# Optimization experiments

Measured on AMD Instinct MI355X. Metric: run time of the kernel, lower is better.

Reference implementation:

```python
import jax, jax.numpy as jnp
import numpy as np

DIM = 512
HEADS = 8
DIM_HEAD = 64
INNER = HEADS * DIM_HEAD  # 512
EPS = 1e-5


def setup_inputs() -> dict:
    key = jax.random.key(0)
    ks = jax.random.split(key, 8)
    b, n = 4, 2048
    x = jax.random.normal(ks[0], (b, n, DIM), dtype=jnp.float32)
    ln_g = jnp.ones((DIM,), jnp.float32)
    ln_b = jnp.zeros((DIM,), jnp.float32)
    w_qkv = jax.random.normal(ks[1], (DIM, 3 * INNER), jnp.float32) * (DIM ** -0.5)
    reattn_w = jax.random.normal(ks[2], (HEADS, HEADS), jnp.float32)
    rn_g = jnp.ones((HEADS,), jnp.float32)
    rn_b = jnp.zeros((HEADS,), jnp.float32)
    w_out = jax.random.normal(ks[3], (INNER, DIM), jnp.float32) * (INNER ** -0.5)
    b_out = jnp.zeros((DIM,), jnp.float32)
    return {"x": x, "ln_g": ln_g, "ln_b": ln_b, "w_qkv": w_qkv,
            "reattn_w": reattn_w, "rn_g": rn_g, "rn_b": rn_b,
            "w_out": w_out, "b_out": b_out}


def _layernorm(x, g, b, axis=-1):
    mu = jnp.mean(x, axis=axis, keepdims=True)
    var = jnp.var(x, axis=axis, keepdims=True)
    return (x - mu) * jax.lax.rsqrt(var + EPS) * g + b


def reference(x, ln_g, ln_b, w_qkv, reattn_w, rn_g, rn_b, w_out, b_out):
    b, n, _ = x.shape
    h, d = HEADS, DIM_HEAD
    scale = d ** -0.5
    xn = _layernorm(x, ln_g, ln_b)                       # [b,n,dim]
    qkv = xn @ w_qkv                                     # [b,n,3*inner]
    q, k, v = jnp.split(qkv, 3, axis=-1)
    to_heads = lambda t: t.reshape(b, n, h, d).transpose(0, 2, 1, 3)  # [b,h,n,d]
    q, k, v = to_heads(q), to_heads(k), to_heads(v)
    dots = jnp.einsum('bhid,bhjd->bhij', q, k) * scale   # [b,h,n,n]
    attn = jax.nn.softmax(dots, axis=-1)
    # cross-head re-attention mixing
    attn = jnp.einsum('bhij,hg->bgij', attn, reattn_w)
    # LayerNorm over the head axis (axis=1), affine params shaped [h]
    attn = _layernorm(attn, rn_g[None, :, None, None], rn_b[None, :, None, None], axis=1)
    out = jnp.einsum('bhij,bhjd->bhid', attn, v)         # [b,h,n,d]
    out = out.transpose(0, 2, 1, 3).reshape(b, n, h * d)
    return out @ w_out + b_out
```

## Files before the change

kernel.cpp:

```cpp
#include <hip/hip_runtime.h>
#include <hip/hip_bf16.h>
#include <math.h>

#define DEV __device__ __forceinline__

typedef short bf16x8 __attribute__((ext_vector_type(8)));
typedef short bf16x4 __attribute__((ext_vector_type(4)));
typedef float f32x4 __attribute__((ext_vector_type(4)));

static const int Nn = 2048;
static const int DIMd = 512;

DEV float bf2f(short u) {
    union { unsigned int i; float f; } c;
    c.i = ((unsigned int)(unsigned short)u) << 16;
    return c.f;
}

DEV short f2bf(float f) {
    union { float f; unsigned int i; } c;
    c.f = f;
    unsigned int u = c.i;
    unsigned int r = (u + 0x7fffu + ((u >> 16) & 1u)) >> 16;
    return (short)r;
}

DEV void gload16(const short* __restrict__ g, short* l) {
    __builtin_amdgcn_global_load_lds(
        (__attribute__((address_space(1))) void*)g,
        (__attribute__((address_space(3))) void*)l, 16, 0, 0);
}

__global__ void k_transpose_cast(const float* __restrict__ src,
                                 short* __restrict__ dst, int K, int N) {
    int o = blockIdx.x * 256 + threadIdx.x;
    if (o >= K * N) return;
    int n = o / K, k = o - n * K;
    dst[o] = f2bf(src[(size_t)k * N + n]);
}

__global__ __launch_bounds__(256) void k_ln(const float* __restrict__ x,
                                            const float* __restrict__ g,
                                            const float* __restrict__ bta,
                                            short* __restrict__ xn) {
    int row = blockIdx.x * 4 + (threadIdx.x >> 6);
    int lane = threadIdx.x & 63;
    const float* xr = x + (size_t)row * DIMd;
    float4 v0 = ((const float4*)xr)[lane * 2];
    float4 v1 = ((const float4*)xr)[lane * 2 + 1];
    float f[8] = {v0.x, v0.y, v0.z, v0.w, v1.x, v1.y, v1.z, v1.w};
    float s = 0.f, sq = 0.f;
#pragma unroll
    for (int t = 0; t < 8; ++t) { s += f[t]; sq += f[t] * f[t]; }
#pragma unroll
    for (int off = 32; off >= 1; off >>= 1) {
        s += __shfl_xor(s, off);
        sq += __shfl_xor(sq, off);
    }
    float mu = s * (1.0f / 512.0f);
    float var = sq * (1.0f / 512.0f) - mu * mu;
    float rs = rsqrtf(var + 1e-5f);
    bf16x8 o;
#pragma unroll
    for (int t = 0; t < 8; ++t) {
        int c = lane * 8 + t;
        o[t] = f2bf((f[t] - mu) * rs * g[c] + bta[c]);
    }
    *(bf16x8*)(xn + (size_t)row * DIMd + lane * 8) = o;
}

DEV void gemm128_loop(const short* __restrict__ A, const short* __restrict__ B,
                      int K, int i0, int n0, int tid,
                      short* As, short* Bs, f32x4 acc[4][4]) {
    const int w = tid >> 6, wr = w >> 1, wc = w & 1;
    const int lane = tid & 63, fr = lane & 15, fq = lane >> 4;
    const int sr = tid >> 3, sc = (tid & 7) * 8;
    for (int k0 = 0; k0 < K; k0 += 64) {
#pragma unroll
        for (int L = 0; L < 4; ++L) {
            gload16(A + (size_t)(i0 + L * 32 + sr) * K + k0 + sc,
                    As + (L * 32 + sr) * 64 + sc);
            gload16(B + (size_t)(n0 + L * 32 + sr) * K + k0 + sc,
                    Bs + (L * 32 + sr) * 64 + sc);
        }
        __syncthreads();
#pragma unroll
        for (int kk = 0; kk < 2; ++kk) {
            bf16x8 af[4], bfr[4];
#pragma unroll
            for (int m = 0; m < 4; ++m)
                af[m] = *(const bf16x8*)(As + (wr * 64 + m * 16 + fr) * 64 + kk * 32 + fq * 8);
#pragma unroll
            for (int n = 0; n < 4; ++n)
                bfr[n] = *(const bf16x8*)(Bs + (wc * 64 + n * 16 + fr) * 64 + kk * 32 + fq * 8);
#pragma unroll
            for (int m = 0; m < 4; ++m)
#pragma unroll
                for (int n = 0; n < 4; ++n)
                    acc[m][n] = __builtin_amdgcn_mfma_f32_16x16x32_bf16(af[m], bfr[n], acc[m][n], 0, 0, 0);
        }
        __syncthreads();
    }
}

__global__ __launch_bounds__(256) void k_qkv(const short* __restrict__ xn,
                                             const short* __restrict__ wT,
                                             short* __restrict__ Q,
                                             short* __restrict__ Kb,
                                             short* __restrict__ Vt) {
    __shared__ short As[128 * 64], Bs[128 * 64];
    int tid = threadIdx.x;
    int i0 = blockIdx.x * 128, n0 = blockIdx.y * 128;
    f32x4 acc[4][4] = {};
    gemm128_loop(xn, wT, DIMd, i0, n0, tid, As, Bs, acc);
    const int w = tid >> 6, wr = w >> 1, wc = w & 1;
    const int lane = tid & 63, fr = lane & 15, fq = lane >> 4;
#pragma unroll
    for (int m = 0; m < 4; ++m) {
#pragma unroll
        for (int n = 0; n < 4; ++n) {
#pragma unroll
            for (int r = 0; r < 4; ++r) {
                int row = i0 + wr * 64 + m * 16 + fq * 4 + r;
                int c = n0 + wc * 64 + n * 16 + fr;
                float v = acc[m][n][r];
                int b = row >> 11, i = row & 2047;
                int t = c >> 9, rem = c & 511;
                int h = rem >> 6, dd = rem & 63;
                size_t bh = (size_t)(b * 8 + h);
                if (t == 0)      Q [(bh * Nn + i) * 64 + dd] = f2bf(v * 0.125f);
                else if (t == 1) Kb[(bh * Nn + i) * 64 + dd] = f2bf(v);
                else             Vt[(bh * 64 + dd) * Nn + i] = f2bf(v);
            }
        }
    }
}

__global__ __launch_bounds__(256) void k_out(const short* __restrict__ outh,
                                             const short* __restrict__ wT,
                                             const float* __restrict__ bias,
                                             float* __restrict__ out) {
    __shared__ short As[128 * 64], Bs[128 * 64];
    int tid = threadIdx.x;
    int i0 = blockIdx.x * 128, n0 = blockIdx.y * 128;
    f32x4 acc[4][4] = {};
    gemm128_loop(outh, wT, 512, i0, n0, tid, As, Bs, acc);
    const int w = tid >> 6, wr = w >> 1, wc = w & 1;
    const int lane = tid & 63, fr = lane & 15, fq = lane >> 4;
#pragma unroll
    for (int m = 0; m < 4; ++m)
#pragma unroll
        for (int n = 0; n < 4; ++n)
#pragma unroll
            for (int r = 0; r < 4; ++r) {
                int row = i0 + wr * 64 + m * 16 + fq * 4 + r;
                int c = n0 + wc * 64 + n * 16 + fr;
                out[(size_t)row * 512 + c] = acc[m][n][r] + bias[c];
            }
}

DEV void decode_bid2(int bid, int& b, int& i0, int& jh) {
    int xcd = bid & 7, slot = bid >> 3;
    b = xcd >> 1;
    jh = xcd & 1;
    i0 = slot * 32;
}

__global__ __launch_bounds__(512)
__attribute__((amdgpu_waves_per_eu(4, 4)))
void k_stats(const short* __restrict__ Q,
             const short* __restrict__ Kb,
             float* __restrict__ mpart,
             float* __restrict__ lpart) {
    int b, i0, jh;
    decode_bid2(blockIdx.x, b, i0, jh);
    int tid = threadIdx.x, wv = tid >> 6, lane = tid & 63;
    int fr = lane & 15, fq = lane >> 4;
    size_t bh = (size_t)(b * 8 + wv);
    const short* qb = Q + (bh * Nn + i0) * 64;
    bf16x8 qf[2][2];
#pragma unroll
    for (int in = 0; in < 2; ++in)
#pragma unroll
        for (int kk = 0; kk < 2; ++kk)
            qf[in][kk] = *(const bf16x8*)(qb + (in * 16 + fr) * 64 + kk * 32 + fq * 8);
    float m[2] = {-1e30f, -1e30f}, l[2] = {0.f, 0.f};
    const short* kbase = Kb + bh * Nn * 64 + (size_t)jh * 1024 * 64;
    for (int jt = 0; jt < 16; ++jt) {
        const short* kb = kbase + jt * 64 * 64;
        f32x4 acc[4][2] = {};
#pragma unroll
        for (int kk = 0; kk < 2; ++kk)
#pragma unroll
            for (int jm = 0; jm < 4; ++jm) {
                bf16x8 kf = *(const bf16x8*)(kb + (jm * 16 + fr) * 64 + kk * 32 + fq * 8);
                acc[jm][0] = __builtin_amdgcn_mfma_f32_16x16x32_bf16(kf, qf[0][kk], acc[jm][0], 0, 0, 0);
                acc[jm][1] = __builtin_amdgcn_mfma_f32_16x16x32_bf16(kf, qf[1][kk], acc[jm][1], 0, 0, 0);
            }
#pragma unroll
        for (int in = 0; in < 2; ++in) {
            float mt = acc[0][in][0];
#pragma unroll
            for (int jm = 0; jm < 4; ++jm)
#pragma unroll
                for (int r = 0; r < 4; ++r) mt = fmaxf(mt, acc[jm][in][r]);
            mt = fmaxf(mt, __shfl_xor(mt, 16));
            mt = fmaxf(mt, __shfl_xor(mt, 32));
            float es = 0.f;
#pragma unroll
            for (int jm = 0; jm < 4; ++jm)
#pragma unroll
                for (int r = 0; r < 4; ++r)
                    es += __expf(acc[jm][in][r] - mt);
            es += __shfl_xor(es, 16);
            es += __shfl_xor(es, 32);
            float mn = fmaxf(m[in], mt);
            l[in] = l[in] * __expf(m[in] - mn) + es * __expf(mt - mn);
            m[in] = mn;
        }
    }
    if (fq == 0) {
#pragma unroll
        for (int in = 0; in < 2; ++in) {
            size_t o = (size_t)jh * 65536 + bh * Nn + i0 + in * 16 + fr;
            mpart[o] = m[in];
            lpart[o] = l[in];
        }
    }
}

__global__ __launch_bounds__(256) void k_zcomb(const float* __restrict__ mpart,
                                               const float* __restrict__ lpart,
                                               float* __restrict__ zstat) {
    int idx = blockIdx.x * 256 + threadIdx.x;
    float m0 = mpart[idx], m1 = mpart[65536 + idx];
    float l0 = lpart[idx], l1 = lpart[65536 + idx];
    float M = fmaxf(m0, m1);
    float L = l0 * __expf(m0 - M) + l1 * __expf(m1 - M);
    zstat[idx] = M + __logf(L);
}

__global__ __launch_bounds__(512)
__attribute__((amdgpu_waves_per_eu(2, 2)))
void k_fused(const short* __restrict__ Q, const short* __restrict__ Kb,
             const short* __restrict__ Vt, const float* __restrict__ zstat,
             const float* __restrict__ R, const float* __restrict__ rg,
             const float* __restrict__ rb, float* __restrict__ opart) {
    __shared__ short S_lds[2][8 * 32 * 64];
    __shared__ short P_lds[2][8 * 32 * 64];
    __shared__ float Rraw[64], Rc[64], rgs[8], rbs[8], zl[8 * 32];
    int b, i0, jh;
    decode_bid2(blockIdx.x, b, i0, jh);
    int tid = threadIdx.x, wv = tid >> 6, lane = tid & 63;
    int fr = lane & 15, fq = lane >> 4;
    if (tid < 64) Rraw[tid] = R[tid];
    if (tid < 8) { rgs[tid] = rg[tid]; rbs[tid] = rb[tid]; }
    if (tid >= 64 && tid < 320) {
        int q = tid - 64;
        zl[q] = zstat[(size_t)(b * 8 + (q >> 5)) * Nn + i0 + (q & 31)];
    }
    __syncthreads();
    if (tid < 64) {
        int h = tid >> 3;
        float mn = 0.f;
#pragma unroll
        for (int gg = 0; gg < 8; ++gg) mn += Rraw[h * 8 + gg];
        Rc[tid] = Rraw[tid] - mn * 0.125f;
    }
    size_t bh = (size_t)(b * 8 + wv);
    const short* qb = Q + (bh * Nn + i0) * 64;
    bf16x8 qf[2][2];
#pragma unroll
    for (int in = 0; in < 2; ++in)
#pragma unroll
        for (int kk = 0; kk < 2; ++kk)
            qf[in][kk] = *(const bf16x8*)(qb + (in * 16 + fr) * 64 + kk * 32 + fq * 8);
    float zh[2] = {zl[wv * 32 + fr], zl[wv * 32 + 16 + fr]};
    const short* kbase = Kb + bh * Nn * 64 + (size_t)jh * 1024 * 64;
    const short* vbase = Vt + bh * 64 * Nn + (size_t)jh * 1024;
    const int mi = tid >> 4, j4 = (tid & 15) * 4;
    const int msw = (mi & 7) << 4;
    f32x4 acc_o[2][4] = {};

    auto phaseA = [&](int jt, char* Sdst) {
        const short* kb = kbase + jt * 64 * 64;
        f32x4 acc[4][2] = {};
#pragma unroll
        for (int kk = 0; kk < 2; ++kk)
#pragma unroll
            for (int jm = 0; jm < 4; ++jm) {
                bf16x8 kf = *(const bf16x8*)(kb + (jm * 16 + fr) * 64 + kk * 32 + fq * 8);
                acc[jm][0] = __builtin_amdgcn_mfma_f32_16x16x32_bf16(kf, qf[0][kk], acc[jm][0], 0, 0, 0);
                acc[jm][1] = __builtin_amdgcn_mfma_f32_16x16x32_bf16(kf, qf[1][kk], acc[jm][1], 0, 0, 0);
            }
#pragma unroll
        for (int in = 0; in < 2; ++in) {
            int i = in * 16 + fr;
            int sw = (i & 7) << 4;
#pragma unroll
            for (int jm = 0; jm < 4; ++jm) {
                bf16x4 pk;
#pragma unroll
                for (int r = 0; r < 4; ++r)
                    pk[r] = f2bf(__expf(acc[jm][in][r] - zh[in]));
                int j0 = jm * 16 + fq * 4;
                *(bf16x4*)(Sdst + wv * 4096 + i * 128 + ((j0 * 2) ^ sw)) = pk;
            }
        }
    };
    auto phaseB = [&](char* Ssrc, char* Pdst) {
        bf16x4 sh[8];
#pragma unroll
        for (int h = 0; h < 8; ++h)
            sh[h] = *(const bf16x4*)(Ssrc + h * 4096 + mi * 128 + ((j4 * 2) ^ msw));
        bf16x4 og[8];
#pragma unroll
        for (int e = 0; e < 4; ++e) {
            float pv[8];
#pragma unroll
            for (int h = 0; h < 8; ++h) pv[h] = bf2f(sh[h][e]);
            float cc[8];
#pragma unroll
            for (int gg = 0; gg < 8; ++gg) {
                float s = 0.f;
#pragma unroll
                for (int h = 0; h < 8; ++h) s += pv[h] * Rc[h * 8 + gg];
                cc[gg] = s;
            }
            float var = 0.f;
#pragma unroll
            for (int gg = 0; gg < 8; ++gg) var += cc[gg] * cc[gg];
            var *= 0.125f;
            float rs_ = rsqrtf(var + 1e-5f);
#pragma unroll
            for (int gg = 0; gg < 8; ++gg)
                og[gg][e] = f2bf(cc[gg] * rs_ * rgs[gg] + rbs[gg]);
        }
#pragma unroll
        for (int gg = 0; gg < 8; ++gg)
            *(bf16x4*)(Pdst + gg * 4096 + mi * 128 + ((j4 * 2) ^ msw)) = og[gg];
    };
    auto phaseC = [&](int jt, char* Psrc) {
        const short* vb = vbase + jt * 64;
#pragma unroll
        for (int kk = 0; kk < 2; ++kk) {
            bf16x8 vf[4];
#pragma unroll
            for (int dn = 0; dn < 4; ++dn)
                vf[dn] = *(const bf16x8*)(vb + (size_t)(dn * 16 + fr) * Nn + kk * 32 + fq * 8);
#pragma unroll
            for (int im = 0; im < 2; ++im) {
                int row = im * 16 + fr;
                bf16x8 pa = *(const bf16x8*)(Psrc + wv * 4096 + row * 128 +
                                             (((kk * 32 + fq * 8) * 2) ^ ((row & 7) << 4)));
#pragma unroll
                for (int dn = 0; dn < 4; ++dn)
                    acc_o[im][dn] = __builtin_amdgcn_mfma_f32_16x16x32_bf16(pa, vf[dn], acc_o[im][dn], 0, 0, 0);
            }
        }
    };

    phaseA(0, (char*)S_lds[0]);
    __syncthreads();
    phaseB((char*)S_lds[0], (char*)P_lds[0]);
    for (int k = 0; k < 16; ++k) {
        __syncthreads();
        phaseC(k, (char*)P_lds[k & 1]);
        if (k < 15) phaseA(k + 1, (char*)S_lds[(k + 1) & 1]);
        __syncthreads();
        if (k < 15) phaseB((char*)S_lds[(k + 1) & 1], (char*)P_lds[(k + 1) & 1]);
    }

    float* po = opart + (size_t)jh * 4194304 + ((size_t)b * Nn + i0) * 512;
#pragma unroll
    for (int im = 0; im < 2; ++im)
#pragma unroll
        for (int dn = 0; dn < 4; ++dn)
#pragma unroll
            for (int r = 0; r < 4; ++r)
                po[(im * 16 + fq * 4 + r) * 512 + wv * 64 + dn * 16 + fr] = acc_o[im][dn][r];
}

__global__ __launch_bounds__(256) void k_osum(const float* __restrict__ opart,
                                              short* __restrict__ outh) {
    int base = (blockIdx.x * 256 + threadIdx.x) * 4;
    f32x4 a = *(const f32x4*)(opart + base);
    f32x4 c = *(const f32x4*)(opart + 4194304 + base);
    bf16x4 o;
#pragma unroll
    for (int t = 0; t < 4; ++t) o[t] = f2bf(a[t] + c[t]);
    *(bf16x4*)(outh + base) = o;
}

extern "C" void kernel_launch(void* const* d_in, const int* in_sizes, int n_in,
                              void* d_out, int out_size, void* d_ws, size_t ws_size,
                              hipStream_t stream) {
    const float* x      = (const float*)d_in[0];
    const float* ln_g   = (const float*)d_in[1];
    const float* ln_b   = (const float*)d_in[2];
    const float* w_qkv  = (const float*)d_in[3];
    const float* reattn = (const float*)d_in[4];
    const float* rn_g   = (const float*)d_in[5];
    const float* rn_b   = (const float*)d_in[6];
    const float* w_out  = (const float*)d_in[7];
    const float* b_out  = (const float*)d_in[8];
    float* out = (float*)d_out;

    char* ws = (char*)d_ws;
    short* wqkvT = (short*)ws; ws += (size_t)1536 * 512 * 2;
    short* woutT = (short*)ws; ws += (size_t)512 * 512 * 2;
    short* xn    = (short*)ws; ws += (size_t)8192 * 512 * 2;
    short* Q     = (short*)ws; ws += (size_t)32 * 2048 * 64 * 2;
    short* Kb    = (short*)ws; ws += (size_t)32 * 2048 * 64 * 2;
    short* Vt    = (short*)ws; ws += (size_t)32 * 64 * 2048 * 2;
    short* outh  = (short*)ws; ws += (size_t)8192 * 512 * 2;
    float* opart = (float*)ws; ws += (size_t)2 * 4194304 * 4;
    float* mpart = (float*)ws; ws += (size_t)2 * 65536 * 4;
    float* lpart = (float*)ws; ws += (size_t)2 * 65536 * 4;
    float* zstat = (float*)xn;

    k_transpose_cast<<<(512 * 1536 + 255) / 256, 256, 0, stream>>>(w_qkv, wqkvT, 512, 1536);
    k_transpose_cast<<<(512 * 512 + 255) / 256, 256, 0, stream>>>(w_out, woutT, 512, 512);
    k_ln<<<8192 / 4, 256, 0, stream>>>(x, ln_g, ln_b, xn);
    k_qkv<<<dim3(8192 / 128, 1536 / 128), 256, 0, stream>>>(xn, wqkvT, Q, Kb, Vt);

    k_stats<<<512, 512, 0, stream>>>(Q, Kb, mpart, lpart);
    k_zcomb<<<256, 256, 0, stream>>>(mpart, lpart, zstat);
    k_fused<<<512, 512, 0, stream>>>(Q, Kb, Vt, zstat, reattn, rn_g, rn_b, opart);
    k_osum<<<4096, 256, 0, stream>>>(opart, outh);

    k_out<<<dim3(8192 / 128, 512 / 128), 256, 0, stream>>>(outh, woutT, b_out, out);
}
```

Measured before the change: 329.2 us.

## Halve fused-attention block to 4 waves, each handling two heads, single-buffer LDS

```diff
diff --git a/kernel.cpp b/kernel.cpp
--- a/kernel.cpp
+++ b/kernel.cpp
@@ -240,25 +240,22 @@
     zstat[idx] = M + __logf(L);
 }
 
-__global__ __launch_bounds__(512)
+__global__ __launch_bounds__(256)
 __attribute__((amdgpu_waves_per_eu(2, 2)))
 void k_fused(const short* __restrict__ Q, const short* __restrict__ Kb,
              const short* __restrict__ Vt, const float* __restrict__ zstat,
              const float* __restrict__ R, const float* __restrict__ rg,
              const float* __restrict__ rb, float* __restrict__ opart) {
-    __shared__ short S_lds[2][8 * 32 * 64];
-    __shared__ short P_lds[2][8 * 32 * 64];
-    __shared__ float Rraw[64], Rc[64], rgs[8], rbs[8], zl[8 * 32];
+    __shared__ short S_lds[8 * 32 * 64];
+    __shared__ short P_lds[8 * 32 * 64];
+    __shared__ float Rraw[64], Rc[64], rgs[8], rbs[8], zl[256];
     int b, i0, jh;
     decode_bid2(blockIdx.x, b, i0, jh);
     int tid = threadIdx.x, wv = tid >> 6, lane = tid & 63;
     int fr = lane & 15, fq = lane >> 4;
     if (tid < 64) Rraw[tid] = R[tid];
     if (tid < 8) { rgs[tid] = rg[tid]; rbs[tid] = rb[tid]; }
-    if (tid >= 64 && tid < 320) {
-        int q = tid - 64;
-        zl[q] = zstat[(size_t)(b * 8 + (q >> 5)) * Nn + i0 + (q & 31)];
-    }
+    zl[tid] = zstat[(size_t)(b * 8 + (tid >> 5)) * Nn + i0 + (tid & 31)];
     __syncthreads();
     if (tid < 64) {
         int h = tid >> 3;
@@ -267,118 +264,138 @@
         for (int gg = 0; gg < 8; ++gg) mn += Rraw[h * 8 + gg];
         Rc[tid] = Rraw[tid] - mn * 0.125f;
     }
-    size_t bh = (size_t)(b * 8 + wv);
-    const short* qb = Q + (bh * Nn + i0) * 64;
-    bf16x8 qf[2][2];
-#pragma unroll
-    for (int in = 0; in < 2; ++in)
-#pragma unroll
-        for (int kk = 0; kk < 2; ++kk)
-            qf[in][kk] = *(const bf16x8*)(qb + (in * 16 + fr) * 64 + kk * 32 + fq * 8);
-    float zh[2] = {zl[wv * 32 + fr], zl[wv * 32 + 16 + fr]};
-    const short* kbase = Kb + bh * Nn * 64 + (size_t)jh * 1024 * 64;
-    const short* vbase = Vt + bh * 64 * Nn + (size_t)jh * 1024;
-    const int mi = tid >> 4, j4 = (tid & 15) * 4;
-    const int msw = (mi & 7) << 4;
-    f32x4 acc_o[2][4] = {};
-
-    auto phaseA = [&](int jt, char* Sdst) {
-        const short* kb = kbase + jt * 64 * 64;
-        f32x4 acc[4][2] = {};
-#pragma unroll
-        for (int kk = 0; kk < 2; ++kk)
-#pragma unroll
-            for (int jm = 0; jm < 4; ++jm) {
-                bf16x8 kf = *(const bf16x8*)(kb + (jm * 16 + fr) * 64 + kk * 32 + fq * 8);
-                acc[jm][0] = __builtin_amdgcn_mfma_f32_16x16x32_bf16(kf, qf[0][kk], acc[jm][0], 0, 0, 0);
-                acc[jm][1] = __builtin_amdgcn_mfma_f32_16x16x32_bf16(kf, qf[1][kk], acc[jm][1], 0, 0, 0);
-            }
-#pragma unroll
-        for (int in = 0; in < 2; ++in) {
-            int i = in * 16 + fr;
-            int sw = (i & 7) << 4;
-#pragma unroll
-            for (int jm = 0; jm < 4; ++jm) {
-                bf16x4 pk;
-#pragma unroll
-                for (int r = 0; r < 4; ++r)
-                    pk[r] = f2bf(__expf(acc[jm][in][r] - zh[in]));
-                int j0 = jm * 16 + fq * 4;
-                *(bf16x4*)(Sdst + wv * 4096 + i * 128 + ((j0 * 2) ^ sw)) = pk;
+    bf16x8 qf[2][2][2];
+    float zh[2][2];
+#pragma unroll
+    for (int hp = 0; hp < 2; ++hp) {
+        int hh = wv + hp * 4;
+        const short* qb = Q + ((size_t)(b * 8 + hh) * Nn + i0) * 64;
+#pragma unroll
+        for (int in = 0; in < 2; ++in)
+#pragma unroll
+            for (int kk = 0; kk < 2; ++kk)
+                qf[hp][in][kk] = *(const bf16x8*)(qb + (in * 16 + fr) * 64 + kk * 32 + fq * 8);
+        zh[hp][0] = zl[hh * 32 + fr];
+        zh[hp][1] = zl[hh * 32 + 16 + fr];
+    }
+    const short* kb0 = Kb + ((size_t)(b * 8 + wv) * Nn + jh * 1024) * 64;
+    const short* kb1 = Kb + ((size_t)(b * 8 + wv + 4) * Nn + jh * 1024) * 64;
+    const short* vb0 = Vt + (size_t)(b * 8 + wv) * 64 * Nn + jh * 1024;
+    const short* vb1 = Vt + (size_t)(b * 8 + wv + 4) * 64 * Nn + jh * 1024;
+    const int mi0 = tid >> 4, j4 = (tid & 15) * 4;
+    const int msw = (mi0 & 7) << 4;
+    f32x4 acc_o[2][2][4] = {};
+
+    auto phaseA = [&](int jt) {
+#pragma unroll
+        for (int hp = 0; hp < 2; ++hp) {
+            const short* kb = (hp ? kb1 : kb0) + jt * 64 * 64;
+            f32x4 acc[4][2] = {};
+#pragma unroll
+            for (int kk = 0; kk < 2; ++kk)
+#pragma unroll
+                for (int jm = 0; jm < 4; ++jm) {
+                    bf16x8 kf = *(const bf16x8*)(kb + (jm * 16 + fr) * 64 + kk * 32 + fq * 8);
+                    acc[jm][0] = __builtin_amdgcn_mfma_f32_16x16x32_bf16(kf, qf[hp][0][kk], acc[jm][0], 0, 0, 0);
+                    acc[jm][1] = __builtin_amdgcn_mfma_f32_16x16x32_bf16(kf, qf[hp][1][kk], acc[jm][1], 0, 0, 0);
+                }
+            char* Sh = (char*)S_lds + (wv + hp * 4) * 4096;
+#pragma unroll
+            for (int in = 0; in < 2; ++in) {
+                int i = in * 16 + fr;
+                int sw = (i & 7) << 4;
+#pragma unroll
+                for (int jm = 0; jm < 4; ++jm) {
+                    bf16x4 pk;
+#pragma unroll
+                    for (int r = 0; r < 4; ++r)
+                        pk[r] = f2bf(__expf(acc[jm][in][r] - zh[hp][in]));
+                    int j0 = jm * 16 + fq * 4;
+                    *(bf16x4*)(Sh + i * 128 + ((j0 * 2) ^ sw)) = pk;
+                }
             }
         }
     };
-    auto phaseB = [&](char* Ssrc, char* Pdst) {
-        bf16x4 sh[8];
-#pragma unroll
-        for (int h = 0; h < 8; ++h)
-            sh[h] = *(const bf16x4*)(Ssrc + h * 4096 + mi * 128 + ((j4 * 2) ^ msw));
-        bf16x4 og[8];
-#pragma unroll
-        for (int e = 0; e < 4; ++e) {
-            float pv[8];
-#pragma unroll
-            for (int h = 0; h < 8; ++h) pv[h] = bf2f(sh[h][e]);
-            float cc[8];
-#pragma unroll
-            for (int gg = 0; gg < 8; ++gg) {
-                float s = 0.f;
-#pragma unroll
-                for (int h = 0; h < 8; ++h) s += pv[h] * Rc[h * 8 + gg];
-                cc[gg] = s;
-            }
-            float var = 0.f;
-#pragma unroll
-            for (int gg = 0; gg < 8; ++gg) var += cc[gg] * cc[gg];
-            var *= 0.125f;
-            float rs_ = rsqrtf(var + 1e-5f);
+    auto phaseB = [&]() {
+#pragma unroll
+        for (int di = 0; di < 32; di += 16) {
+            int mi = mi0 + di;
+            bf16x4 sh[8];
+#pragma unroll
+            for (int h = 0; h < 8; ++h)
+                sh[h] = *(const bf16x4*)((char*)S_lds + h * 4096 + mi * 128 + ((j4 * 2) ^ msw));
+            bf16x4 og[8];
+#pragma unroll
+            for (int e = 0; e < 4; ++e) {
+                float pv[8];
+#pragma unroll
+                for (int h = 0; h < 8; ++h) pv[h] = bf2f(sh[h][e]);
+                float cc[8];
+#pragma unroll
+                for (int gg = 0; gg < 8; ++gg) {
+                    float s = 0.f;
+#pragma unroll
+                    for (int h = 0; h < 8; ++h) s += pv[h] * Rc[h * 8 + gg];
+                    cc[gg] = s;
+                }
+                float var = 0.f;
+#pragma unroll
+                for (int gg = 0; gg < 8; ++gg) var += cc[gg] * cc[gg];
+                var *= 0.125f;
+                float rs_ = rsqrtf(var + 1e-5f);
+#pragma unroll
+                for (int gg = 0; gg < 8; ++gg)
+                    og[gg][e] = f2bf(cc[gg] * rs_ * rgs[gg] + rbs[gg]);
+            }
 #pragma unroll
             for (int gg = 0; gg < 8; ++gg)
-                og[gg][e] = f2bf(cc[gg] * rs_ * rgs[gg] + rbs[gg]);
-        }
-#pragma unroll
-        for (int gg = 0; gg < 8; ++gg)
-            *(bf16x4*)(Pdst + gg * 4096 + mi * 128 + ((j4 * 2) ^ msw)) = og[gg];
+                *(bf16x4*)((char*)P_lds + gg * 4096 + mi * 128 + ((j4 * 2) ^ msw)) = og[gg];
+        }
     };
-    auto phaseC = [&](int jt, char* Psrc) {
-        const short* vb = vbase + jt * 64;
-#pragma unroll
-        for (int kk = 0; kk < 2; ++kk) {
-            bf16x8 vf[4];
-#pragma unroll
-            for (int dn = 0; dn < 4; ++dn)
-                vf[dn] = *(const bf16x8*)(vb + (size_t)(dn * 16 + fr) * Nn + kk * 32 + fq * 8);
-#pragma unroll
-            for (int im = 0; im < 2; ++im) {
-                int row = im * 16 + fr;
-                bf16x8 pa = *(const bf16x8*)(Psrc + wv * 4096 + row * 128 +
-                                             (((kk * 32 + fq * 8) * 2) ^ ((row & 7) << 4)));
+    auto phaseC = [&](int jt) {
+#pragma unroll
+        for (int hp = 0; hp < 2; ++hp) {
+            const short* vb = (hp ? vb1 : vb0) + jt * 64;
+            char* Ph = (char*)P_lds + (wv + hp * 4) * 4096;
+#pragma unroll
+            for (int kk = 0; kk < 2; ++kk) {
+                bf16x8 vf[4];
 #pragma unroll
                 for (int dn = 0; dn < 4; ++dn)
-                    acc_o[im][dn] = __builtin_amdgcn_mfma_f32_16x16x32_bf16(pa, vf[dn], acc_o[im][dn], 0, 0, 0);
+                    vf[dn] = *(const bf16x8*)(vb + (size_t)(dn * 16 + fr) * Nn + kk * 32 + fq * 8);
+#pragma unroll
+                for (int im = 0; im < 2; ++im) {
+                    int row = im * 16 + fr;
+                    bf16x8 pa = *(const bf16x8*)(Ph + row * 128 +
+                                                 (((kk * 32 + fq * 8) * 2) ^ ((row & 7) << 4)));
+#pragma unroll
+                    for (int dn = 0; dn < 4; ++dn)
+                        acc_o[hp][im][dn] = __builtin_amdgcn_mfma_f32_16x16x32_bf16(pa, vf[dn], acc_o[hp][im][dn], 0, 0, 0);
+                }
             }
         }
     };
 
-    phaseA(0, (char*)S_lds[0]);
-    __syncthreads();
-    phaseB((char*)S_lds[0], (char*)P_lds[0]);
+    phaseA(0);
     for (int k = 0; k < 16; ++k) {
         __syncthreads();
-        phaseC(k, (char*)P_lds[k & 1]);
-        if (k < 15) phaseA(k + 1, (char*)S_lds[(k + 1) & 1]);
+        phaseB();
         __syncthreads();
-        if (k < 15) phaseB((char*)S_lds[(k + 1) & 1], (char*)P_lds[(k + 1) & 1]);
+        phaseC(k);
+        if (k < 15) phaseA(k + 1);
     }
 
     float* po = opart + (size_t)jh * 4194304 + ((size_t)b * Nn + i0) * 512;
 #pragma unroll
-    for (int im = 0; im < 2; ++im)
-#pragma unroll
-        for (int dn = 0; dn < 4; ++dn)
-#pragma unroll
-            for (int r = 0; r < 4; ++r)
-                po[(im * 16 + fq * 4 + r) * 512 + wv * 64 + dn * 16 + fr] = acc_o[im][dn][r];
+    for (int hp = 0; hp < 2; ++hp)
+#pragma unroll
+        for (int im = 0; im < 2; ++im)
+#pragma unroll
+            for (int dn = 0; dn < 4; ++dn)
+#pragma unroll
+                for (int r = 0; r < 4; ++r)
+                    po[(im * 16 + fq * 4 + r) * 512 + (wv + hp * 4) * 64 + dn * 16 + fr] =
+                        acc_o[hp][im][dn][r];
 }
 
 __global__ __launch_bounds__(256) void k_osum(const float* __restrict__ opart,
@@ -426,7 +443,7 @@
 
     k_stats<<<512, 512, 0, stream>>>(Q, Kb, mpart, lpart);
     k_zcomb<<<256, 256, 0, stream>>>(mpart, lpart, zstat);
-    k_fused<<<512, 512, 0, stream>>>(Q, Kb, Vt, zstat, reattn, rn_g, rn_b, opart);
+    k_fused<<<512, 256, 0, stream>>>(Q, Kb, Vt, zstat, reattn, rn_g, rn_b, opart);
     k_osum<<<4096, 256, 0, stream>>>(opart, outh);
 
     k_out<<<dim3(8192 / 128, 512 / 128), 256, 0, stream>>>(outh, woutT, b_out, out);
```

After: 307.1 us, median of 2. 6.7% less time.
